# Optimization experiments

Hardware: AMD Instinct MI355X
Metric: run time of the kernel (lower is better)

The kernel has to match this reference:

```python
import jax, jax.numpy as jnp
import numpy as np

T_TEST, B, F, H, N_OUT = 8192, 8, 100, 512, 1


def setup_inputs() -> dict:
    key = jax.random.key(0)
    ks = jax.random.split(key, 7)
    s = 0.05  # keep generated-weight magnitudes in a realistic hypernetwork range
    return {
        "x_test": jax.random.normal(ks[0], (T_TEST, B, F), dtype=jnp.float32),
        "w1": jax.random.normal(ks[1], (B, F, H), dtype=jnp.float32) * s,
        "b1": jax.random.normal(ks[2], (B, H), dtype=jnp.float32) * s,
        "w2": jax.random.normal(ks[3], (B, H, H), dtype=jnp.float32) * s,
        "b2": jax.random.normal(ks[4], (B, H), dtype=jnp.float32) * s,
        "w3": jax.random.normal(ks[5], (B, H, N_OUT), dtype=jnp.float32) * s,
        "b3": jax.random.normal(ks[6], (B, N_OUT), dtype=jnp.float32) * s,
    }


def reference(x_test, w1, b1, w2, b2, w3, b3):
    # MotherNet.nn_forward with predicted_activation='relu',
    # weight_embedding_rank=None, low_rank_last=False.
    # Original torch: h = (x.unsqueeze(-1) * w.unsqueeze(0)).sum(2) + b
    # == per-dataset batched GEMM over the B axis.
    x = jnp.nan_to_num(x_test)                    # [T, B, F]
    h = jnp.einsum('tbf,bfh->tbh', x, w1) + b1    # [T, B, H]
    h = jax.nn.relu(h)
    h = jnp.einsum('tbf,bfh->tbh', h, w2) + b2    # [T, B, H]
    h = jax.nn.relu(h)
    h = jnp.einsum('tbf,bfh->tbh', h, w3) + b3    # [T, B, 1]
    return h
```

## Files before the change

### kernel.cpp

```cpp
#include <hip/hip_runtime.h>

#define T_TEST 8192
#define BB 8
#define FF 100
#define HH 512

typedef __bf16 bf16x8 __attribute__((ext_vector_type(8)));
typedef float f32x16 __attribute__((ext_vector_type(16)));
typedef unsigned short u16;
typedef unsigned int u32;

__device__ __forceinline__ u16 f2bf(float f) {
    u32 u = __float_as_uint(f);
    u += 0x7fffu + ((u >> 16) & 1);
    return (u16)(u >> 16);
}

__device__ __forceinline__ float nan2num(float v) {
    u32 u = __float_as_uint(v);
    if ((u & 0x7f800000u) == 0x7f800000u) {
        v = (u & 0x007fffffu) ? 0.f : ((u >> 31) ? -3.3895314e38f : 3.3895314e38f);
    }
    return v;
}

__global__ void prep_w(const float* __restrict__ w1, const float* __restrict__ w2,
                       u16* __restrict__ w1f, u16* __restrict__ w2f) {
    int bid = blockIdx.x;
    if (bid < 256) {
        int t = bid * 256 + threadIdx.x;
        int lane = t & 63;
        int n32 = (t >> 6) & 15;
        int b = t >> 13;
        int n = n32 * 32 + (lane & 31);
        int kb = ((t >> 10) & 7) * 16 + (lane >> 5) * 8;
        u32 p[4];
#pragma unroll
        for (int jp = 0; jp < 4; ++jp) {
            int k0 = kb + jp * 2;
            float v0 = (k0 < FF)     ? w1[(b * FF + k0) * HH + n]     : 0.f;
            float v1 = (k0 + 1 < FF) ? w1[(b * FF + k0 + 1) * HH + n] : 0.f;
            p[jp] = (u32)f2bf(v0) | ((u32)f2bf(v1) << 16);
        }
        uint4 o = {p[0], p[1], p[2], p[3]};
        *(uint4*)(w1f + (size_t)t * 8) = o;
    } else {
        int t = (bid - 256) * 256 + threadIdx.x;
        int lane = t & 63;
        int n32 = (t >> 6) & 15;
        int b = t >> 15;
        int n = n32 * 32 + (lane & 31);
        int kb = ((t >> 10) & 31) * 16 + (lane >> 5) * 8;
        u32 p[4];
#pragma unroll
        for (int jp = 0; jp < 4; ++jp) {
            int k0 = kb + jp * 2;
            float v0 = w2[(b * HH + k0) * HH + n];
            float v1 = w2[(b * HH + k0 + 1) * HH + n];
            p[jp] = (u32)f2bf(v0) | ((u32)f2bf(v1) << 16);
        }
        uint4 o = {p[0], p[1], p[2], p[3]};
        *(uint4*)(w2f + (size_t)t * 8) = o;
    }
}

__global__ __launch_bounds__(512, 4) void fused_mlp(
    const float* __restrict__ x, const u16* __restrict__ w1f,
    const float* __restrict__ b1, const u16* __restrict__ w2f,
    const float* __restrict__ b2, const float* __restrict__ w3,
    const float* __restrict__ b3, float* __restrict__ out) {
    __shared__ __align__(16) char lds[81920];
    u16* xf  = (u16*)lds;
    u16* h1f = (u16*)(lds + 16384);

    const int tid = threadIdx.x;
    const int b = blockIdx.x;
    const int m0 = blockIdx.y * 64;
    const int lane = tid & 63;
    const int ws = __builtin_amdgcn_readfirstlane(tid >> 6);
    const int l31 = lane & 31, lh = lane >> 5;
    const int n32b = ws * 2;
    const int r2 = ws * 4;

    const bf16x8* W1 = (const bf16x8*)w1f + (size_t)b * 8192;
    const bf16x8* W2 = (const bf16x8*)w2f + (size_t)b * 32768;

    bf16x8 pa[2][2], pb[4][2];

#pragma unroll
    for (int s = 0; s < 4; ++s)
#pragma unroll
        for (int ni = 0; ni < 2; ++ni)
            pb[s][ni] = W1[(s * 16 + n32b + ni) * 64 + lane];

    float b1v[2];
    b1v[0] = b1[b * HH + (n32b + 0) * 32 + l31];
    b1v[1] = b1[b * HH + (n32b + 1) * 32 + l31];

    if (ws < 7) {
        int row = lane, s = ws;
        int mi = row >> 5, m = row & 31;
        const float* xr = x + ((size_t)(m0 + row) * BB + b) * FF + s * 16;
        u32 p[8];
#pragma unroll
        for (int i = 0; i < 8; ++i) p[i] = 0;
        if (s <= 5) {
#pragma unroll
            for (int j = 0; j < 4; ++j) {
                float4 v = *(const float4*)(xr + j * 4);
                p[j * 2 + 0] = (u32)f2bf(nan2num(v.x)) | ((u32)f2bf(nan2num(v.y)) << 16);
                p[j * 2 + 1] = (u32)f2bf(nan2num(v.z)) | ((u32)f2bf(nan2num(v.w)) << 16);
            }
        } else {
            float4 v = *(const float4*)(xr);
            p[0] = (u32)f2bf(nan2num(v.x)) | ((u32)f2bf(nan2num(v.y)) << 16);
            p[1] = (u32)f2bf(nan2num(v.z)) | ((u32)f2bf(nan2num(v.w)) << 16);
        }
        int fi1 = s * 2 + mi;
        uint4 g0 = {p[0], p[1], p[2], p[3]};
        uint4 g1 = {p[4], p[5], p[6], p[7]};
        *(uint4*)(xf + (fi1 * 64 + m) * 8)      = g0;
        *(uint4*)(xf + (fi1 * 64 + 32 + m) * 8) = g1;
    }
    __syncthreads();

    f32x16 acc1[2][2] = {};
#pragma unroll
    for (int s = 0; s < 2; ++s)
#pragma unroll
        for (int mi = 0; mi < 2; ++mi)
            pa[s][mi] = *(const bf16x8*)(xf + ((s * 2 + mi) * 64 + lane) * 8);
#pragma unroll
    for (int ks = 0; ks < 7; ++ks) {
        const int pA = ks & 1, pB = ks & 3;
        bf16x8 a0 = pa[pA][0], a1 = pa[pA][1];
        bf16x8 b0 = pb[pB][0], b1r = pb[pB][1];
        if (ks < 5) {
#pragma unroll
            for (int mi = 0; mi < 2; ++mi)
                pa[pA][mi] = *(const bf16x8*)(xf + (((ks + 2) * 2 + mi) * 64 + lane) * 8);
        }
        if (ks < 3) {
#pragma unroll
            for (int ni = 0; ni < 2; ++ni)
                pb[pB][ni] = W1[((ks + 4) * 16 + n32b + ni) * 64 + lane];
        }
        acc1[0][0] = __builtin_amdgcn_mfma_f32_32x32x16_bf16(a0, b0,  acc1[0][0], 0, 0, 0);
        acc1[0][1] = __builtin_amdgcn_mfma_f32_32x32x16_bf16(a0, b1r, acc1[0][1], 0, 0, 0);
        acc1[1][0] = __builtin_amdgcn_mfma_f32_32x32x16_bf16(a1, b0,  acc1[1][0], 0, 0, 0);
        acc1[1][1] = __builtin_amdgcn_mfma_f32_32x32x16_bf16(a1, b1r, acc1[1][1], 0, 0, 0);
    }

#pragma unroll
    for (int s = 0; s < 4; ++s) {
        int k = (r2 + s) & 31;
#pragma unroll
        for (int ni = 0; ni < 2; ++ni)
            pb[s][ni] = W2[(k * 16 + n32b + ni) * 64 + lane];
    }

    {
        char* hw = (char*)h1f + (l31 >> 4) * 2048 + ((l31 >> 3) & 1) * 512 +
                   (l31 & 6) * 2 + lh * 64 + n32b * 4096;
#pragma unroll
        for (int ni = 0; ni < 2; ++ni) {
#pragma unroll
            for (int mi = 0; mi < 2; ++mi)
#pragma unroll
                for (int qd = 0; qd < 4; ++qd) {
                    u32 own01 = (u32)f2bf(fmaxf(acc1[mi][ni][qd * 4 + 0] + b1v[ni], 0.f)) |
                                ((u32)f2bf(fmaxf(acc1[mi][ni][qd * 4 + 1] + b1v[ni], 0.f)) << 16);
                    u32 own23 = (u32)f2bf(fmaxf(acc1[mi][ni][qd * 4 + 2] + b1v[ni], 0.f)) |
                                ((u32)f2bf(fmaxf(acc1[mi][ni][qd * 4 + 3] + b1v[ni], 0.f)) << 16);
                    u32 oth01 = __shfl_xor(own01, 1, 64);
                    u32 oth23 = __shfl_xor(own23, 1, 64);
                    char* base = hw + ni * 4096 + mi * 1024 + qd * 128;
                    if (!(lane & 1)) {
                        *(u32*)(base +  0) = (own01 & 0xffffu) | (oth01 << 16);
                        *(u32*)(base + 16) = (own01 >> 16) | (oth01 & 0xffff0000u);
                    } else {
                        *(u32*)(base + 32) = (oth23 & 0xffffu) | (own23 << 16);
                        *(u32*)(base + 48) = (oth23 >> 16) | (own23 & 0xffff0000u);
                    }
                }
        }
    }
    __syncthreads();

    float b2v[2], w3v[2];
#pragma unroll
    for (int ni = 0; ni < 2; ++ni) {
        int n = (n32b + ni) * 32 + l31;
        b2v[ni] = b2[b * HH + n];
        w3v[ni] = w3[b * HH + n];
    }

    f32x16 acc2[2][2] = {};
    const char* hv  = (const char*)h1f + r2 * 2048 + (size_t)lane * 16;
    const char* hvB = hv - 65536;
#pragma unroll
    for (int s = 0; s < 2; ++s) {
        const char* hp = (s + r2 < 32) ? hv : hvB;
#pragma unroll
        for (int mi = 0; mi < 2; ++mi)
            pa[s][mi] = *(const bf16x8*)(hp + s * 2048 + mi * 1024);
    }
#pragma unroll
    for (int ks = 0; ks < 32; ++ks) {
        const int pA = ks & 1, pB = ks & 3;
        bf16x8 a0 = pa[pA][0], a1 = pa[pA][1];
        bf16x8 b0 = pb[pB][0], b1r = pb[pB][1];
        if (ks < 30) {
            const char* hp = (ks + 2 + r2 < 32) ? hv : hvB;
#pragma unroll
            for (int mi = 0; mi < 2; ++mi)
                pa[pA][mi] = *(const bf16x8*)(hp + (ks + 2) * 2048 + mi * 1024);
        }
        if (ks < 28) {
            int kspf = ks + 4 + r2;
            kspf -= (kspf >= 32) ? 32 : 0;
#pragma unroll
            for (int ni = 0; ni < 2; ++ni)
                pb[pB][ni] = W2[(kspf * 16 + n32b + ni) * 64 + lane];
        }
        acc2[0][0] = __builtin_amdgcn_mfma_f32_32x32x16_bf16(a0, b0,  acc2[0][0], 0, 0, 0);
        acc2[0][1] = __builtin_amdgcn_mfma_f32_32x32x16_bf16(a0, b1r, acc2[0][1], 0, 0, 0);
        acc2[1][0] = __builtin_amdgcn_mfma_f32_32x32x16_bf16(a1, b0,  acc2[1][0], 0, 0, 0);
        acc2[1][1] = __builtin_amdgcn_mfma_f32_32x32x16_bf16(a1, b1r, acc2[1][1], 0, 0, 0);
    }

    float* part = (float*)xf;
#pragma unroll
    for (int mi = 0; mi < 2; ++mi)
#pragma unroll
        for (int r = 0; r < 16; ++r) {
            float v = fmaxf(acc2[mi][0][r] + b2v[0], 0.f) * w3v[0] +
                      fmaxf(acc2[mi][1][r] + b2v[1], 0.f) * w3v[1];
            v += __shfl_xor(v, 1, 64);
            v += __shfl_xor(v, 2, 64);
            v += __shfl_xor(v, 4, 64);
            v += __shfl_xor(v, 8, 64);
            v += __shfl_xor(v, 16, 64);
            if (l31 == 0)
                part[ws * 64 + mi * 32 + (r & 3) + 8 * (r >> 2) + 4 * lh] = v;
        }
    __syncthreads();
    if (tid < 64) {
        float s = b3[b];
#pragma unroll
        for (int ww = 0; ww < 8; ++ww) s += part[ww * 64 + tid];
        out[(size_t)(m0 + tid) * BB + b] = s;
    }
}

extern "C" void kernel_launch(void* const* d_in, const int* in_sizes, int n_in,
                              void* d_out, int out_size, void* d_ws, size_t ws_size,
                              hipStream_t stream) {
    const float* x  = (const float*)d_in[0];
    const float* w1 = (const float*)d_in[1];
    const float* b1 = (const float*)d_in[2];
    const float* w2 = (const float*)d_in[3];
    const float* b2 = (const float*)d_in[4];
    const float* w3 = (const float*)d_in[5];
    const float* b3 = (const float*)d_in[6];
    float* out = (float*)d_out;

    u16* w1f = (u16*)d_ws;
    u16* w2f = w1f + (size_t)BB * 8192 * 8;

    prep_w<<<1280, 256, 0, stream>>>(w1, w2, w1f, w2f);

    fused_mlp<<<dim3(BB, T_TEST / 64), 512, 0, stream>>>(
        x, w1f, b1, w2f, b2, w3, b3, out);
}
```

Baseline: 137.1 us.

## Split fused MLP into layer-1 kernel and layer-2/3 kernel via global h1

Result: slower. 156.7 us (+14.3%).

```diff
diff --git a/kernel.cpp b/kernel.cpp
--- a/kernel.cpp
+++ b/kernel.cpp
@@ -64,11 +64,9 @@
     }
 }
 
-__global__ __launch_bounds__(512, 4) void fused_mlp(
+__global__ __launch_bounds__(512, 2) void l1_kernel(
     const float* __restrict__ x, const u16* __restrict__ w1f,
-    const float* __restrict__ b1, const u16* __restrict__ w2f,
-    const float* __restrict__ b2, const float* __restrict__ w3,
-    const float* __restrict__ b3, float* __restrict__ out) {
+    const float* __restrict__ b1, u16* __restrict__ h1g) {
     __shared__ __align__(16) char lds[81920];
     u16* xf  = (u16*)lds;
     u16* h1f = (u16*)(lds + 16384);
@@ -80,10 +78,8 @@
     const int ws = __builtin_amdgcn_readfirstlane(tid >> 6);
     const int l31 = lane & 31, lh = lane >> 5;
     const int n32b = ws * 2;
-    const int r2 = ws * 4;
 
     const bf16x8* W1 = (const bf16x8*)w1f + (size_t)b * 8192;
-    const bf16x8* W2 = (const bf16x8*)w2f + (size_t)b * 32768;
 
     bf16x8 pa[2][2], pb[4][2];
 
@@ -149,14 +145,6 @@
         acc1[0][1] = __builtin_amdgcn_mfma_f32_32x32x16_bf16(a0, b1r, acc1[0][1], 0, 0, 0);
         acc1[1][0] = __builtin_amdgcn_mfma_f32_32x32x16_bf16(a1, b0,  acc1[1][0], 0, 0, 0);
         acc1[1][1] = __builtin_amdgcn_mfma_f32_32x32x16_bf16(a1, b1r, acc1[1][1], 0, 0, 0);
-    }
-
-#pragma unroll
-    for (int s = 0; s < 4; ++s) {
-        int k = (r2 + s) & 31;
-#pragma unroll
-        for (int ni = 0; ni < 2; ++ni)
-            pb[s][ni] = W2[(k * 16 + n32b + ni) * 64 + lane];
     }
 
     {
@@ -187,6 +175,41 @@
     }
     __syncthreads();
 
+    {
+        const uint4* src = (const uint4*)h1f;
+        uint4* dst = (uint4*)(h1g + (size_t)(b * 128 + blockIdx.y) * 32768);
+#pragma unroll
+        for (int j = 0; j < 8; ++j)
+            dst[tid + j * 512] = src[tid + j * 512];
+    }
+}
+
+__global__ __launch_bounds__(512, 4) void l23_kernel(
+    const u16* __restrict__ h1g, const u16* __restrict__ w2f,
+    const float* __restrict__ b2, const float* __restrict__ w3,
+    const float* __restrict__ b3, float* __restrict__ out) {
+    __shared__ float part[512];
+
+    const int tid = threadIdx.x;
+    const int b = blockIdx.x;
+    const int m0 = blockIdx.y * 64;
+    const int lane = tid & 63;
+    const int ws = __builtin_amdgcn_readfirstlane(tid >> 6);
+    const int l31 = lane & 31, lh = lane >> 5;
+    const int n32b = ws * 2;
+
+    const bf16x8* W2 = (const bf16x8*)w2f + (size_t)b * 32768;
+    const char* Ab = (const char*)(h1g + (size_t)(b * 128 + blockIdx.y) * 32768) +
+                     (size_t)lane * 16;
+
+    bf16x8 pa[2][2], pb[4][2];
+
+#pragma unroll
+    for (int s = 0; s < 4; ++s)
+#pragma unroll
+        for (int ni = 0; ni < 2; ++ni)
+            pb[s][ni] = W2[(s * 16 + n32b + ni) * 64 + lane];
+
     float b2v[2], w3v[2];
 #pragma unroll
     for (int ni = 0; ni < 2; ++ni) {
@@ -195,33 +218,27 @@
         w3v[ni] = w3[b * HH + n];
     }
 
+#pragma unroll
+    for (int s = 0; s < 2; ++s)
+#pragma unroll
+        for (int mi = 0; mi < 2; ++mi)
+            pa[s][mi] = *(const bf16x8*)(Ab + (s * 2 + mi) * 1024);
+
     f32x16 acc2[2][2] = {};
-    const char* hv  = (const char*)h1f + r2 * 2048 + (size_t)lane * 16;
-    const char* hvB = hv - 65536;
-#pragma unroll
-    for (int s = 0; s < 2; ++s) {
-        const char* hp = (s + r2 < 32) ? hv : hvB;
-#pragma unroll
-        for (int mi = 0; mi < 2; ++mi)
-            pa[s][mi] = *(const bf16x8*)(hp + s * 2048 + mi * 1024);
-    }
 #pragma unroll
     for (int ks = 0; ks < 32; ++ks) {
         const int pA = ks & 1, pB = ks & 3;
         bf16x8 a0 = pa[pA][0], a1 = pa[pA][1];
         bf16x8 b0 = pb[pB][0], b1r = pb[pB][1];
         if (ks < 30) {
-            const char* hp = (ks + 2 + r2 < 32) ? hv : hvB;
 #pragma unroll
             for (int mi = 0; mi < 2; ++mi)
-                pa[pA][mi] = *(const bf16x8*)(hp + (ks + 2) * 2048 + mi * 1024);
+                pa[pA][mi] = *(const bf16x8*)(Ab + ((ks + 2) * 2 + mi) * 1024);
         }
         if (ks < 28) {
-            int kspf = ks + 4 + r2;
-            kspf -= (kspf >= 32) ? 32 : 0;
 #pragma unroll
             for (int ni = 0; ni < 2; ++ni)
-                pb[pB][ni] = W2[(kspf * 16 + n32b + ni) * 64 + lane];
+                pb[pB][ni] = W2[((ks + 4) * 16 + n32b + ni) * 64 + lane];
         }
         acc2[0][0] = __builtin_amdgcn_mfma_f32_32x32x16_bf16(a0, b0,  acc2[0][0], 0, 0, 0);
         acc2[0][1] = __builtin_amdgcn_mfma_f32_32x32x16_bf16(a0, b1r, acc2[0][1], 0, 0, 0);
@@ -229,7 +246,6 @@
         acc2[1][1] = __builtin_amdgcn_mfma_f32_32x32x16_bf16(a1, b1r, acc2[1][1], 0, 0, 0);
     }
 
-    float* part = (float*)xf;
 #pragma unroll
     for (int mi = 0; mi < 2; ++mi)
 #pragma unroll
@@ -267,9 +283,9 @@
 
     u16* w1f = (u16*)d_ws;
     u16* w2f = w1f + (size_t)BB * 8192 * 8;
+    u16* h1g = w2f + (size_t)BB * 32768 * 8;
 
     prep_w<<<1280, 256, 0, stream>>>(w1, w2, w1f, w2f);
-
-    fused_mlp<<<dim3(BB, T_TEST / 64), 512, 0, stream>>>(
-        x, w1f, b1, w2f, b2, w3, b3, out);
-}
+    l1_kernel<<<dim3(BB, T_TEST / 64), 512, 0, stream>>>(x, w1f, b1, h1g);
+    l23_kernel<<<dim3(BB, T_TEST / 64), 512, 0, stream>>>(h1g, w2f, b2, w3, b3, out);
+}
```

## Halve row tile per block to 32 rows, shrinking LDS and raising occupancy

Applied to the files above, without the earlier changes.

New measurement: 142.3 us. +3.8%, slower.

```diff
diff --git a/kernel.cpp b/kernel.cpp
--- a/kernel.cpp
+++ b/kernel.cpp
@@ -64,18 +64,18 @@
     }
 }
 
-__global__ __launch_bounds__(512, 4) void fused_mlp(
+__global__ __launch_bounds__(512, 6) void fused_mlp(
     const float* __restrict__ x, const u16* __restrict__ w1f,
     const float* __restrict__ b1, const u16* __restrict__ w2f,
     const float* __restrict__ b2, const float* __restrict__ w3,
     const float* __restrict__ b3, float* __restrict__ out) {
-    __shared__ __align__(16) char lds[81920];
+    __shared__ __align__(16) char lds[40960];
     u16* xf  = (u16*)lds;
-    u16* h1f = (u16*)(lds + 16384);
+    u16* h1f = (u16*)(lds + 8192);
 
     const int tid = threadIdx.x;
     const int b = blockIdx.x;
-    const int m0 = blockIdx.y * 64;
+    const int m0 = blockIdx.y * 32;
     const int lane = tid & 63;
     const int ws = __builtin_amdgcn_readfirstlane(tid >> 6);
     const int l31 = lane & 31, lh = lane >> 5;
@@ -85,10 +85,10 @@
     const bf16x8* W1 = (const bf16x8*)w1f + (size_t)b * 8192;
     const bf16x8* W2 = (const bf16x8*)w2f + (size_t)b * 32768;
 
-    bf16x8 pa[2][2], pb[4][2];
-
-#pragma unroll
-    for (int s = 0; s < 4; ++s)
+    bf16x8 pa[2], pb[2][2];
+
+#pragma unroll
+    for (int s = 0; s < 2; ++s)
 #pragma unroll
         for (int ni = 0; ni < 2; ++ni)
             pb[s][ni] = W1[(s * 16 + n32b + ni) * 64 + lane];
@@ -97,62 +97,53 @@
     b1v[0] = b1[b * HH + (n32b + 0) * 32 + l31];
     b1v[1] = b1[b * HH + (n32b + 1) * 32 + l31];
 
-    if (ws < 7) {
-        int row = lane, s = ws;
-        int mi = row >> 5, m = row & 31;
-        const float* xr = x + ((size_t)(m0 + row) * BB + b) * FF + s * 16;
-        u32 p[8];
-#pragma unroll
-        for (int i = 0; i < 8; ++i) p[i] = 0;
-        if (s <= 5) {
-#pragma unroll
-            for (int j = 0; j < 4; ++j) {
-                float4 v = *(const float4*)(xr + j * 4);
-                p[j * 2 + 0] = (u32)f2bf(nan2num(v.x)) | ((u32)f2bf(nan2num(v.y)) << 16);
-                p[j * 2 + 1] = (u32)f2bf(nan2num(v.z)) | ((u32)f2bf(nan2num(v.w)) << 16);
+    {
+        int row = tid & 31, s = tid >> 5;
+        if (s < 7) {
+            const float* xr = x + ((size_t)(m0 + row) * BB + b) * FF + s * 16;
+            u32 p[8];
+#pragma unroll
+            for (int i = 0; i < 8; ++i) p[i] = 0;
+            if (s <= 5) {
+#pragma unroll
+                for (int j = 0; j < 4; ++j) {
+                    float4 v = *(const float4*)(xr + j * 4);
+                    p[j * 2 + 0] = (u32)f2bf(nan2num(v.x)) | ((u32)f2bf(nan2num(v.y)) << 16);
+                    p[j * 2 + 1] = (u32)f2bf(nan2num(v.z)) | ((u32)f2bf(nan2num(v.w)) << 16);
+                }
+            } else {
+                float4 v = *(const float4*)(xr);
+                p[0] = (u32)f2bf(nan2num(v.x)) | ((u32)f2bf(nan2num(v.y)) << 16);
+                p[1] = (u32)f2bf(nan2num(v.z)) | ((u32)f2bf(nan2num(v.w)) << 16);
             }
-        } else {
-            float4 v = *(const float4*)(xr);
-            p[0] = (u32)f2bf(nan2num(v.x)) | ((u32)f2bf(nan2num(v.y)) << 16);
-            p[1] = (u32)f2bf(nan2num(v.z)) | ((u32)f2bf(nan2num(v.w)) << 16);
-        }
-        int fi1 = s * 2 + mi;
-        uint4 g0 = {p[0], p[1], p[2], p[3]};
-        uint4 g1 = {p[4], p[5], p[6], p[7]};
-        *(uint4*)(xf + (fi1 * 64 + m) * 8)      = g0;
-        *(uint4*)(xf + (fi1 * 64 + 32 + m) * 8) = g1;
+            uint4 g0 = {p[0], p[1], p[2], p[3]};
+            uint4 g1 = {p[4], p[5], p[6], p[7]};
+            *(uint4*)(xf + (s * 64 + row) * 8)      = g0;
+            *(uint4*)(xf + (s * 64 + 32 + row) * 8) = g1;
+        }
     }
     __syncthreads();
 
-    f32x16 acc1[2][2] = {};
-#pragma unroll
-    for (int s = 0; s < 2; ++s)
-#pragma unroll
-        for (int mi = 0; mi < 2; ++mi)
-            pa[s][mi] = *(const bf16x8*)(xf + ((s * 2 + mi) * 64 + lane) * 8);
+    f32x16 acc1[2] = {};
+    pa[0] = *(const bf16x8*)(xf + (0 * 64 + lane) * 8);
+    pa[1] = *(const bf16x8*)(xf + (1 * 64 + lane) * 8);
 #pragma unroll
     for (int ks = 0; ks < 7; ++ks) {
-        const int pA = ks & 1, pB = ks & 3;
-        bf16x8 a0 = pa[pA][0], a1 = pa[pA][1];
-        bf16x8 b0 = pb[pB][0], b1r = pb[pB][1];
+        const int p = ks & 1;
+        bf16x8 a0 = pa[p];
+        bf16x8 b0 = pb[p][0], b1r = pb[p][1];
         if (ks < 5) {
-#pragma unroll
-            for (int mi = 0; mi < 2; ++mi)
-                pa[pA][mi] = *(const bf16x8*)(xf + (((ks + 2) * 2 + mi) * 64 + lane) * 8);
-        }
-        if (ks < 3) {
+            pa[p] = *(const bf16x8*)(xf + ((ks + 2) * 64 + lane) * 8);
 #pragma unroll
             for (int ni = 0; ni < 2; ++ni)
-                pb[pB][ni] = W1[((ks + 4) * 16 + n32b + ni) * 64 + lane];
-        }
-        acc1[0][0] = __builtin_amdgcn_mfma_f32_32x32x16_bf16(a0, b0,  acc1[0][0], 0, 0, 0);
-        acc1[0][1] = __builtin_amdgcn_mfma_f32_32x32x16_bf16(a0, b1r, acc1[0][1], 0, 0, 0);
-        acc1[1][0] = __builtin_amdgcn_mfma_f32_32x32x16_bf16(a1, b0,  acc1[1][0], 0, 0, 0);
-        acc1[1][1] = __builtin_amdgcn_mfma_f32_32x32x16_bf16(a1, b1r, acc1[1][1], 0, 0, 0);
-    }
-
-#pragma unroll
-    for (int s = 0; s < 4; ++s) {
+                pb[p][ni] = W1[((ks + 2) * 16 + n32b + ni) * 64 + lane];
+        }
+        acc1[0] = __builtin_amdgcn_mfma_f32_32x32x16_bf16(a0, b0,  acc1[0], 0, 0, 0);
+        acc1[1] = __builtin_amdgcn_mfma_f32_32x32x16_bf16(a0, b1r, acc1[1], 0, 0, 0);
+    }
+
+#pragma unroll
+    for (int s = 0; s < 2; ++s) {
         int k = (r2 + s) & 31;
 #pragma unroll
         for (int ni = 0; ni < 2; ++ni)
@@ -160,29 +151,27 @@
     }
 
     {
-        char* hw = (char*)h1f + (l31 >> 4) * 2048 + ((l31 >> 3) & 1) * 512 +
-                   (l31 & 6) * 2 + lh * 64 + n32b * 4096;
+        char* hw = (char*)h1f + n32b * 2048 + (l31 >> 4) * 1024 +
+                   ((l31 >> 3) & 1) * 512 + (l31 & 6) * 2 + lh * 64;
 #pragma unroll
         for (int ni = 0; ni < 2; ++ni) {
 #pragma unroll
-            for (int mi = 0; mi < 2; ++mi)
-#pragma unroll
-                for (int qd = 0; qd < 4; ++qd) {
-                    u32 own01 = (u32)f2bf(fmaxf(acc1[mi][ni][qd * 4 + 0] + b1v[ni], 0.f)) |
-                                ((u32)f2bf(fmaxf(acc1[mi][ni][qd * 4 + 1] + b1v[ni], 0.f)) << 16);
-                    u32 own23 = (u32)f2bf(fmaxf(acc1[mi][ni][qd * 4 + 2] + b1v[ni], 0.f)) |
-                                ((u32)f2bf(fmaxf(acc1[mi][ni][qd * 4 + 3] + b1v[ni], 0.f)) << 16);
-                    u32 oth01 = __shfl_xor(own01, 1, 64);
-                    u32 oth23 = __shfl_xor(own23, 1, 64);
-                    char* base = hw + ni * 4096 + mi * 1024 + qd * 128;
-                    if (!(lane & 1)) {
-                        *(u32*)(base +  0) = (own01 & 0xffffu) | (oth01 << 16);
-                        *(u32*)(base + 16) = (own01 >> 16) | (oth01 & 0xffff0000u);
-                    } else {
-                        *(u32*)(base + 32) = (oth23 & 0xffffu) | (own23 << 16);
-                        *(u32*)(base + 48) = (oth23 >> 16) | (own23 & 0xffff0000u);
-                    }
+            for (int qd = 0; qd < 4; ++qd) {
+                u32 own01 = (u32)f2bf(fmaxf(acc1[ni][qd * 4 + 0] + b1v[ni], 0.f)) |
+                            ((u32)f2bf(fmaxf(acc1[ni][qd * 4 + 1] + b1v[ni], 0.f)) << 16);
+                u32 own23 = (u32)f2bf(fmaxf(acc1[ni][qd * 4 + 2] + b1v[ni], 0.f)) |
+                            ((u32)f2bf(fmaxf(acc1[ni][qd * 4 + 3] + b1v[ni], 0.f)) << 16);
+                u32 oth01 = __shfl_xor(own01, 1, 64);
+                u32 oth23 = __shfl_xor(own23, 1, 64);
+                char* base = hw + ni * 2048 + qd * 128;
+                if (!(lane & 1)) {
+                    *(u32*)(base +  0) = (own01 & 0xffffu) | (oth01 << 16);
+                    *(u32*)(base + 16) = (own01 >> 16) | (oth01 & 0xffff0000u);
+                } else {
+                    *(u32*)(base + 32) = (oth23 & 0xffffu) | (own23 << 16);
+                    *(u32*)(base + 48) = (oth23 >> 16) | (own23 & 0xffff0000u);
                 }
+            }
         }
     }
     __syncthreads();
@@ -195,60 +184,50 @@
         w3v[ni] = w3[b * HH + n];
     }
 
-    f32x16 acc2[2][2] = {};
-    const char* hv  = (const char*)h1f + r2 * 2048 + (size_t)lane * 16;
-    const char* hvB = hv - 65536;
+    f32x16 acc2[2] = {};
+    const char* hv  = (const char*)h1f + r2 * 1024 + (size_t)lane * 16;
+    const char* hvB = hv - 32768;
 #pragma unroll
     for (int s = 0; s < 2; ++s) {
         const char* hp = (s + r2 < 32) ? hv : hvB;
-#pragma unroll
-        for (int mi = 0; mi < 2; ++mi)
-            pa[s][mi] = *(const bf16x8*)(hp + s * 2048 + mi * 1024);
+        pa[s] = *(const bf16x8*)(hp + s * 1024);
     }
 #pragma unroll
     for (int ks = 0; ks < 32; ++ks) {
-        const int pA = ks & 1, pB = ks & 3;
-        bf16x8 a0 = pa[pA][0], a1 = pa[pA][1];
-        bf16x8 b0 = pb[pB][0], b1r = pb[pB][1];
+        const int p = ks & 1;
+        bf16x8 a0 = pa[p];
+        bf16x8 b0 = pb[p][0], b1r = pb[p][1];
         if (ks < 30) {
             const char* hp = (ks + 2 + r2 < 32) ? hv : hvB;
-#pragma unroll
-            for (int mi = 0; mi < 2; ++mi)
-                pa[pA][mi] = *(const bf16x8*)(hp + (ks + 2) * 2048 + mi * 1024);
-        }
-        if (ks < 28) {
-            int kspf = ks + 4 + r2;
+            pa[p] = *(const bf16x8*)(hp + (ks + 2) * 1024);
+            int kspf = ks + 2 + r2;
             kspf -= (kspf >= 32) ? 32 : 0;
 #pragma unroll
             for (int ni = 0; ni < 2; ++ni)
-                pb[pB][ni] = W2[(kspf * 16 + n32b + ni) * 64 + lane];
-        }
-        acc2[0][0] = __builtin_amdgcn_mfma_f32_32x32x16_bf16(a0, b0,  acc2[0][0], 0, 0, 0);
-        acc2[0][1] = __builtin_amdgcn_mfma_f32_32x32x16_bf16(a0, b1r, acc2[0][1], 0, 0, 0);
-        acc2[1][0] = __builtin_amdgcn_mfma_f32_32x32x16_bf16(a1, b0,  acc2[1][0], 0, 0, 0);
-        acc2[1][1] = __builtin_amdgcn_mfma_f32_32x32x16_bf16(a1, b1r, acc2[1][1], 0, 0, 0);
+                pb[p][ni] = W2[(kspf * 16 + n32b + ni) * 64 + lane];
+        }
+        acc2[0] = __builtin_amdgcn_mfma_f32_32x32x16_bf16(a0, b0,  acc2[0], 0, 0, 0);
+        acc2[1] = __builtin_amdgcn_mfma_f32_32x32x16_bf16(a0, b1r, acc2[1], 0, 0, 0);
     }
 
     float* part = (float*)xf;
 #pragma unroll
-    for (int mi = 0; mi < 2; ++mi)
-#pragma unroll
-        for (int r = 0; r < 16; ++r) {
-            float v = fmaxf(acc2[mi][0][r] + b2v[0], 0.f) * w3v[0] +
-                      fmaxf(acc2[mi][1][r] + b2v[1], 0.f) * w3v[1];
-            v += __shfl_xor(v, 1, 64);
-            v += __shfl_xor(v, 2, 64);
-            v += __shfl_xor(v, 4, 64);
-            v += __shfl_xor(v, 8, 64);
-            v += __shfl_xor(v, 16, 64);
-            if (l31 == 0)
-                part[ws * 64 + mi * 32 + (r & 3) + 8 * (r >> 2) + 4 * lh] = v;
-        }
+    for (int r = 0; r < 16; ++r) {
+        float v = fmaxf(acc2[0][r] + b2v[0], 0.f) * w3v[0] +
+                  fmaxf(acc2[1][r] + b2v[1], 0.f) * w3v[1];
+        v += __shfl_xor(v, 1, 64);
+        v += __shfl_xor(v, 2, 64);
+        v += __shfl_xor(v, 4, 64);
+        v += __shfl_xor(v, 8, 64);
+        v += __shfl_xor(v, 16, 64);
+        if (l31 == 0)
+            part[ws * 32 + (r & 3) + 8 * (r >> 2) + 4 * lh] = v;
+    }
     __syncthreads();
-    if (tid < 64) {
+    if (tid < 32) {
         float s = b3[b];
 #pragma unroll
-        for (int ww = 0; ww < 8; ++ww) s += part[ww * 64 + tid];
+        for (int ww = 0; ww < 8; ++ww) s += part[ww * 32 + tid];
         out[(size_t)(m0 + tid) * BB + b] = s;
     }
 }
@@ -270,6 +249,6 @@
 
     prep_w<<<1280, 256, 0, stream>>>(w1, w2, w1f, w2f);
 
-    fused_mlp<<<dim3(BB, T_TEST / 64), 512, 0, stream>>>(
+    fused_mlp<<<dim3(BB, T_TEST / 32), 512, 0, stream>>>(
         x, w1f, b1, w2f, b2, w3, b3, out);
 }
```
